# Performance work log

Hardware: AMD Instinct MI355X
Metric: run time of the kernel (lower is better)

## Reference

```python
import jax, jax.numpy as jnp
import numpy as np

B, T, E, H, V = 128, 400, 128, 128, 50000
H2, H4, H6 = 2 * H, 4 * H, 6 * H


def setup_inputs() -> dict:
    key = jax.random.key(0)
    ks = jax.random.split(key, 16)
    s = 0.05
    return dict(
        input_ids=jax.random.randint(ks[0], (B, 1), 0, V),
        pre_hidden=jax.random.normal(ks[1], (1, B, H2), jnp.float32),
        pre_cell=jax.random.normal(ks[2], (1, B, H2), jnp.float32),
        enc_outputs=jax.random.normal(ks[3], (B, T, H2), jnp.float32),
        source_input=jax.random.randint(ks[4], (B, T), 0, V),
        coverage=jax.random.uniform(ks[5], (B, 1, T), jnp.float32),
        emb_table=s * jax.random.normal(ks[6], (V, E), jnp.float32),
        w_ih=s * jax.random.normal(ks[7], (4 * H2, E), jnp.float32),
        w_hh=s * jax.random.normal(ks[8], (4 * H2, H2), jnp.float32),
        b_ih=jnp.zeros((4 * H2,), jnp.float32),
        b_hh=jnp.zeros((4 * H2,), jnp.float32),
        w_align=s * jax.random.normal(ks[9], (1, H6), jnp.float32),
        b_align=jnp.zeros((1,), jnp.float32),
        w_cov=s * jax.random.normal(ks[10], (H2, 1), jnp.float32),
        b_cov=jnp.zeros((H2,), jnp.float32),
        w_fc1=s * jax.random.normal(ks[11], (H4, H4), jnp.float32),
        b_fc1=jnp.zeros((H4,), jnp.float32),
        w_fc2=s * jax.random.normal(ks[12], (V, H4), jnp.float32),
        b_fc2=jnp.zeros((V,), jnp.float32),
        w_gen=s * jax.random.normal(ks[13], (1, H4 + E), jnp.float32),
        b_gen=jnp.zeros((1,), jnp.float32),
    )


def reference(input_ids, pre_hidden, pre_cell, enc_outputs, source_input, coverage,
              emb_table, w_ih, w_hh, b_ih, b_hh, w_align, b_align, w_cov, b_cov,
              w_fc1, b_fc1, w_fc2, b_fc2, w_gen, b_gen):
    # embedding lookup (flag=False path: no dropout)
    emb = emb_table[input_ids[:, 0]]                      # [B,E]
    # single-step LSTM (PyTorch gate order i,f,g,o; hidden size 2H)
    h0, c0 = pre_hidden[0], pre_cell[0]                   # [B,2H]
    gates = emb @ w_ih.T + b_ih + h0 @ w_hh.T + b_hh      # [B,8H]
    i, f, g, o = jnp.split(gates, 4, axis=-1)
    c = jax.nn.sigmoid(f) * c0 + jax.nn.sigmoid(i) * jnp.tanh(g)
    h = jax.nn.sigmoid(o) * jnp.tanh(c)                   # [B,2H]
    # coverage feature + attention over encoder steps
    cov_feat = coverage.transpose(0, 2, 1) @ w_cov.T + b_cov        # [B,T,2H]
    h_rep = jnp.broadcast_to(h[:, None, :], enc_outputs.shape)     # [B,T,2H]
    combine = jnp.concatenate([enc_outputs, h_rep, cov_feat], -1)  # [B,T,6H]
    scores = jnp.tanh(combine @ w_align.T + b_align)               # [B,T,1]
    attn = jax.nn.softmax(scores, axis=1)                          # [B,T,1]
    attn_bt = attn[:, :, 0]                                        # [B,T]
    cov_bt = coverage[:, 0, :]
    cov_loss = jnp.sum(jnp.minimum(attn_bt, cov_bt))
    new_cov = coverage + attn_bt[:, None, :]                       # [B,1,T]
    # context + vocab distribution
    context = jnp.einsum('bt,bte->be', attn_bt, enc_outputs)       # [B,2H]
    fc = jnp.tanh(jnp.concatenate([h, context], -1) @ w_fc1.T + b_fc1)
    pvocab = jax.nn.softmax(fc @ w_fc2.T + b_fc2, axis=1)          # [B,V]
    # copy distribution: fused batched scatter-add (replaces per-batch one-hot matmul loop)
    b_idx = jnp.arange(attn_bt.shape[0])[:, None]
    copy = jnp.zeros_like(pvocab).at[b_idx, source_input].add(attn_bt)
    # generation probability and mixture
    gen_in = jnp.concatenate([context, h, emb], -1)                # [B,4H+E]
    pgen = jax.nn.sigmoid(gen_in @ w_gen.T + b_gen)                # [B,1]
    out = pvocab * pgen + copy * (1.0 - pgen)
    return (out, h[None], c[None], attn_bt[:, None, :], copy, new_cov, cov_loss)
```

## Files before the change

kernel.cpp:

```cpp
#include <hip/hip_runtime.h>
#include <hip/hip_bf16.h>
#include <math.h>

#define B_  128
#define T_  400
#define E_  128
#define H2_ 256
#define H4_ 512
#define V_  50000
#define G4_ 1024
#define KACT 384
#define NTILE 1563

#define OFF_H       6400000
#define OFF_C       6432768
#define OFF_ATTN    6465536
#define OFF_COPY    6516736
#define OFF_NEWCOV 12916736
#define OFF_COVLOSS 12967936

#define WS_ACT   0
#define WS_GATES (WS_ACT + KACT*B_)
#define WS_HC    (WS_GATES + G4_*B_)
#define WS_FCB   (WS_HC + H4_*B_)
#define WS_SC    (WS_FCB + H4_*B_/2)
#define WS_ATTN  (WS_SC + B_*T_)
#define WS_CTXP  (WS_ATTN + B_*T_)
#define WS_SMP   (WS_CTXP + B_*8*H2_)
#define WS_HDOT  (WS_SMP + B_*8*2)
#define WS_COVP  (WS_HDOT + B_)
#define WS_PGEN  (WS_COVP + B_)
#define WS_MAX   (WS_PGEN + B_)
#define WS_INV   (WS_MAX + B_)
#define WS_AB    (WS_INV + B_)

typedef __attribute__((ext_vector_type(8))) short bf16x8;
typedef __attribute__((ext_vector_type(4))) float f32x4;
typedef __attribute__((ext_vector_type(16))) float f32x16;

__device__ inline float sigmoidf_(float x){ return 1.f/(1.f+__expf(-x)); }

__device__ inline short f2bf(float x){
  __hip_bfloat16 h = __float2bfloat16(x);
  return *reinterpret_cast<short*>(&h);
}

__device__ inline float blk_reduce_sum(float v, float* red){
  int t = threadIdx.x;
  red[t] = v; __syncthreads();
  for (int s = 128; s > 0; s >>= 1){ if (t < s) red[t] += red[t+s]; __syncthreads(); }
  float r = red[0]; __syncthreads(); return r;
}
__device__ inline float blk_reduce_max(float v, float* red){
  int t = threadIdx.x;
  red[t] = v; __syncthreads();
  for (int s = 128; s > 0; s >>= 1){ if (t < s) red[t] = fmaxf(red[t], red[t+s]); __syncthreads(); }
  float r = red[0]; __syncthreads(); return r;
}

__global__ __launch_bounds__(256) void k_zero(float* __restrict__ p){
  size_t i = ((size_t)blockIdx.x*256 + threadIdx.x)*4;
  if (i < (size_t)B_*V_)
    *(float4*)&p[i] = make_float4(0.f,0.f,0.f,0.f);
}

__global__ __launch_bounds__(256) void k_act(const int* __restrict__ ids,
    const float* __restrict__ pre_h, const float* __restrict__ emb_table,
    const float* __restrict__ w_align, const float* __restrict__ w_cov,
    const float* __restrict__ b_cov, float* __restrict__ act,
    float* __restrict__ ab){
  __shared__ float red[256];
  int t = threadIdx.x;
  int idx = blockIdx.x*256 + t;
  int k = idx >> 7, b = idx & 127;
  float v = (k < E_) ? emb_table[(size_t)ids[b]*E_ + k]
                     : pre_h[b*H2_ + (k - E_)];
  act[idx] = v;
  if (blockIdx.x == 0) {
    float wa = w_align[2*H2_ + t];
    float alpha = blk_reduce_sum(w_cov[t]*wa, red);
    float beta  = blk_reduce_sum(b_cov[t]*wa, red);
    if (t == 0) { ab[0] = alpha; ab[1] = beta; }
  }
}

__global__ __launch_bounds__(256) void k_gates(const float* __restrict__ act,
    const float* __restrict__ w_ih, const float* __restrict__ w_hh,
    const float* __restrict__ b_ih, const float* __restrict__ b_hh,
    float* __restrict__ gates){
  __shared__ float wt[8][KACT];
  int t = threadIdx.x; int j0 = blockIdx.x*8;
  for (int idx = t; idx < 8*KACT; idx += 256) {
    int r = idx / KACT, k = idx % KACT;
    int j = j0 + r;
    wt[r][k] = (k < E_) ? w_ih[j*E_ + k] : w_hh[j*H2_ + (k - E_)];
  }
  __syncthreads();
  int jq = t >> 7, b = t & 127;
  float acc[4] = {0.f,0.f,0.f,0.f};
  for (int k = 0; k < KACT; ++k) {
    float a = act[k*B_ + b];
    #pragma unroll
    for (int jj = 0; jj < 4; ++jj) acc[jj] += wt[jq*4+jj][k]*a;
  }
  #pragma unroll
  for (int jj = 0; jj < 4; ++jj) {
    int j = j0 + jq*4 + jj;
    gates[j*B_ + b] = acc[jj] + b_ih[j] + b_hh[j];
  }
}

__global__ __launch_bounds__(256) void k_lstm(const float* __restrict__ gates,
    const float* __restrict__ pre_c, const float* __restrict__ w_align,
    float* __restrict__ o_h, float* __restrict__ o_c,
    float* __restrict__ hc, float* __restrict__ hdot){
  __shared__ float red[256];
  int b = blockIdx.x, k = threadIdx.x;
  float i_ = gates[(0*H2_ + k)*B_ + b];
  float f_ = gates[(1*H2_ + k)*B_ + b];
  float g_ = gates[(2*H2_ + k)*B_ + b];
  float o_ = gates[(3*H2_ + k)*B_ + b];
  float c = sigmoidf_(f_)*pre_c[b*H2_ + k] + sigmoidf_(i_)*tanhf(g_);
  float h = sigmoidf_(o_)*tanhf(c);
  o_h[b*H2_ + k] = h;
  o_c[b*H2_ + k] = c;
  hc[k*B_ + b] = h;
  float s = blk_reduce_sum(h * w_align[H2_ + k], red);
  if (k == 0) hdot[b] = s;
}

__global__ __launch_bounds__(256) void k_scores(const float* __restrict__ enc,
    const float* __restrict__ cov, const float* __restrict__ w_align,
    const float* __restrict__ b_align, const float* __restrict__ hdot,
    const float* __restrict__ ab, float* __restrict__ sc){
  int b = blockIdx.y, c = blockIdx.x;
  int t = threadIdx.x, wave = t >> 6, lane = t & 63;
  float4 wa4 = *(const float4*)&w_align[lane*4];
  float hd = hdot[b], alpha = ab[0], beta = ab[1], ba = b_align[0];
  int t0 = c*50;
  for (int tt = t0 + wave; tt < t0 + 50; tt += 4) {
    const float4* ep = (const float4*)&enc[((size_t)b*T_ + tt)*H2_];
    float4 e4 = ep[lane];
    float d = e4.x*wa4.x + e4.y*wa4.y + e4.z*wa4.z + e4.w*wa4.w;
    #pragma unroll
    for (int m = 32; m >= 1; m >>= 1) d += __shfl_xor(d, m);
    if (lane == 0)
      sc[b*T_ + tt] = tanhf(d + hd + alpha*cov[b*T_ + tt] + beta + ba);
  }
}

__global__ __launch_bounds__(256) void k_soft(const float* __restrict__ sc_in,
    const float* __restrict__ cov, const int* __restrict__ src,
    float* __restrict__ o_attn, float* __restrict__ o_newcov,
    float* __restrict__ o_copy, float* __restrict__ covp,
    float* __restrict__ attn_ws){
  __shared__ float red[256];
  int b = blockIdx.x, t = threadIdx.x;
  float x1 = sc_in[b*T_ + t];
  float x2 = (t + 256 < T_) ? sc_in[b*T_ + t + 256] : -1e30f;
  float mx = blk_reduce_max(fmaxf(x1, x2), red);
  float e1 = __expf(x1 - mx);
  float e2 = (t + 256 < T_) ? __expf(x2 - mx) : 0.f;
  float sum = blk_reduce_sum(e1 + e2, red);
  float inv = 1.f/sum;
  float cl;
  {
    float a1 = e1*inv; float c1 = cov[b*T_ + t];
    attn_ws[b*T_ + t] = a1;
    o_attn[b*T_ + t] = a1;
    o_newcov[b*T_ + t] = c1 + a1;
    atomicAdd(&o_copy[(size_t)b*V_ + src[b*T_ + t]], a1);
    cl = fminf(a1, c1);
  }
  if (t + 256 < T_) {
    float a2 = e2*inv; float c2 = cov[b*T_ + t + 256];
    attn_ws[b*T_ + t + 256] = a2;
    o_attn[b*T_ + t + 256] = a2;
    o_newcov[b*T_ + t + 256] = c2 + a2;
    atomicAdd(&o_copy[(size_t)b*V_ + src[b*T_ + t + 256]], a2);
    cl += fminf(a2, c2);
  }
  float clsum = blk_reduce_sum(cl, red);
  if (t == 0) covp[b] = clsum;
}

__global__ __launch_bounds__(256) void k_ctx(const float* __restrict__ enc,
    const float* __restrict__ attn_ws, float* __restrict__ ctxp){
  __shared__ float a_s[50];
  int b = blockIdx.y, c = blockIdx.x, e = threadIdx.x;
  int t0 = c*50;
  if (e < 50) a_s[e] = attn_ws[b*T_ + t0 + e];
  __syncthreads();
  float acc = 0.f;
  #pragma unroll 5
  for (int i = 0; i < 50; ++i)
    acc += a_s[i] * enc[((size_t)b*T_ + t0 + i)*H2_ + e];
  ctxp[((size_t)b*8 + c)*H2_ + e] = acc;
}

__global__ __launch_bounds__(256) void k_ctxpgen(const float* __restrict__ ctxp,
    const int* __restrict__ ids, const float* __restrict__ emb_table,
    const float* __restrict__ w_gen, const float* __restrict__ b_gen,
    float* __restrict__ hc, float* __restrict__ pgen){
  __shared__ float red[256];
  int b = blockIdx.x, t = threadIdx.x;
  float ctx = 0.f;
  #pragma unroll
  for (int c = 0; c < 8; ++c) ctx += ctxp[((size_t)b*8 + c)*H2_ + t];
  hc[(H2_ + t)*B_ + b] = ctx;
  float p = ctx*w_gen[t] + hc[t*B_ + b]*w_gen[H2_ + t];
  if (t < E_) p += emb_table[(size_t)ids[b]*E_ + t]*w_gen[2*H2_ + t];
  float s = blk_reduce_sum(p, red);
  if (t == 0) pgen[b] = sigmoidf_(s + b_gen[0]);
}

__global__ __launch_bounds__(256) void k_fc1(const float* __restrict__ hc,
    const float* __restrict__ w_fc1, const float* __restrict__ b_fc1,
    short* __restrict__ fcb){
  __shared__ float wt[16][H4_];
  int t = threadIdx.x; int j0 = blockIdx.x*16;
  for (int idx = t; idx < 16*H4_; idx += 256) {
    int r = idx >> 9, k = idx & 511;
    wt[r][k] = w_fc1[(j0 + r)*H4_ + k];
  }
  __syncthreads();
  int jq = t >> 7, b = t & 127;
  float acc[8] = {};
  for (int k = 0; k < H4_; ++k) {
    float a = hc[k*B_ + b];
    #pragma unroll
    for (int jj = 0; jj < 8; ++jj) acc[jj] += wt[jq*8+jj][k]*a;
  }
  bf16x8 pack;
  #pragma unroll
  for (int jj = 0; jj < 8; ++jj) {
    int j = j0 + jq*8 + jj;
    pack[jj] = f2bf(tanhf(acc[jj] + b_fc1[j]));
  }
  *(bf16x8*)&fcb[(size_t)b*H4_ + j0 + jq*8] = pack;
}

__global__ __launch_bounds__(256, 1) void k_gemv(const short* __restrict__ fcb,
    const float* __restrict__ w_fc2, const float* __restrict__ b_fc2,
    float* __restrict__ logits){
  __shared__ __attribute__((aligned(16))) char lds[131072];
  int t = threadIdx.x;
  int w = t >> 6, l = t & 63;
  int ln = l & 31, g2 = l >> 5;

  #pragma unroll
  for (int i = 0; i < 32; ++i) {
    int s = i*256 + t;
    int c = s >> 9, r = (s & 511) >> 2, sg = s & 3;
    bf16x8 d = *(const bf16x8*)&fcb[r*H4_ + c*32 + sg*8];
    *(bf16x8*)(lds + c*8192 + sg*2048 + (((r ^ (sg << 1)) & 127)*16)) = d;
  }
  __syncthreads();

  int wgid = blockIdx.x*4 + w;
  for (int tile = wgid; tile < NTILE; tile += 1024) {
    int v = tile*32 + ln;
    int vc = v < V_ ? v : V_ - 1;
    const float* wr = w_fc2 + (size_t)vc*H4_ + g2*8;
    f32x16 acc0 = {}, acc1 = {}, acc2 = {}, acc3 = {};
    #pragma unroll 8
    for (int ks = 0; ks < 32; ++ks) {
      float4 f0 = *(const float4*)(wr + ks*16);
      float4 f1 = *(const float4*)(wr + ks*16 + 4);
      bf16x8 bf;
      bf[0]=f2bf(f0.x); bf[1]=f2bf(f0.y); bf[2]=f2bf(f0.z); bf[3]=f2bf(f0.w);
      bf[4]=f2bf(f1.x); bf[5]=f2bf(f1.y); bf[6]=f2bf(f1.z); bf[7]=f2bf(f1.w);
      int sg = (ks & 1)*2 + g2;
      char* base = lds + (ks >> 1)*8192 + sg*2048;
      bf16x8 a0 = *(const bf16x8*)(base + ((( 0 + ln) ^ (sg << 1)) & 127)*16);
      bf16x8 a1 = *(const bf16x8*)(base + (((32 + ln) ^ (sg << 1)) & 127)*16);
      bf16x8 a2 = *(const bf16x8*)(base + (((64 + ln) ^ (sg << 1)) & 127)*16);
      bf16x8 a3 = *(const bf16x8*)(base + (((96 + ln) ^ (sg << 1)) & 127)*16);
      acc0 = __builtin_amdgcn_mfma_f32_32x32x16_bf16(a0, bf, acc0, 0, 0, 0);
      acc1 = __builtin_amdgcn_mfma_f32_32x32x16_bf16(a1, bf, acc1, 0, 0, 0);
      acc2 = __builtin_amdgcn_mfma_f32_32x32x16_bf16(a2, bf, acc2, 0, 0, 0);
      acc3 = __builtin_amdgcn_mfma_f32_32x32x16_bf16(a3, bf, acc3, 0, 0, 0);
    }
    if (v < V_) {
      float bias = b_fc2[v];
      #pragma unroll
      for (int r = 0; r < 16; ++r) {
        int brow = (r & 3) + 8*(r >> 2) + 4*g2;
        logits[(size_t)(brow)*V_ + v]      = acc0[r] + bias;
        logits[(size_t)(32 + brow)*V_ + v] = acc1[r] + bias;
        logits[(size_t)(64 + brow)*V_ + v] = acc2[r] + bias;
        logits[(size_t)(96 + brow)*V_ + v] = acc3[r] + bias;
      }
    }
  }
}

__global__ __launch_bounds__(256) void k_smp(const float* __restrict__ logits,
    float* __restrict__ smp){
  __shared__ float rm[256], rs[256];
  int b = blockIdx.y, c = blockIdx.x, t = threadIdx.x;
  int v0 = c*6250, v1 = v0 + 6250;
  float m = -1e30f, s = 0.f;
  for (int v = v0 + t; v < v1; v += 256) {
    float x = logits[(size_t)b*V_ + v];
    float nm = fmaxf(m, x);
    s = s*__expf(m - nm) + __expf(x - nm);
    m = nm;
  }
  rm[t] = m; rs[t] = s; __syncthreads();
  for (int k = 128; k > 0; k >>= 1) {
    if (t < k) {
      float m1 = rm[t], s1 = rs[t], m2 = rm[t+k], s2 = rs[t+k];
      float nm = fmaxf(m1, m2);
      rm[t] = nm; rs[t] = s1*__expf(m1-nm) + s2*__expf(m2-nm);
    }
    __syncthreads();
  }
  if (t == 0) { smp[(b*8+c)*2] = rm[0]; smp[(b*8+c)*2+1] = rs[0]; }
}

__global__ __launch_bounds__(128) void k_smred_cl(const float* __restrict__ smp,
    const float* __restrict__ covp, float* __restrict__ mx,
    float* __restrict__ inv, float* __restrict__ o_cl){
  __shared__ float red[128];
  int t = threadIdx.x;
  float m = -1e30f, s = 0.f;
  #pragma unroll
  for (int c = 0; c < 8; ++c) {
    float m2 = smp[(t*8+c)*2], s2 = smp[(t*8+c)*2+1];
    float nm = fmaxf(m, m2);
    s = s*__expf(m - nm) + s2*__expf(m2 - nm);
    m = nm;
  }
  mx[t] = m; inv[t] = 1.f/s;
  red[t] = covp[t]; __syncthreads();
  for (int k = 64; k > 0; k >>= 1){ if (t < k) red[t] += red[t+k]; __syncthreads(); }
  if (t == 0) o_cl[0] = red[0];
}

__global__ __launch_bounds__(256) void k_final(const float* __restrict__ copy,
    const float* __restrict__ mx, const float* __restrict__ inv_s,
    const float* __restrict__ pgen, float* __restrict__ out){
  size_t gid = (size_t)blockIdx.x*256 + threadIdx.x;
  int b = (int)(gid / (V_/4));
  int v = (int)(gid % (V_/4))*4;
  size_t idx = (size_t)b*V_ + v;
  float m = mx[b], is = inv_s[b], pg = pgen[b];
  float4 lg = *(const float4*)&out[idx];
  float4 cp = *(const float4*)&copy[idx];
  float4 o;
  o.x = __expf(lg.x - m)*is*pg + cp.x*(1.f - pg);
  o.y = __expf(lg.y - m)*is*pg + cp.y*(1.f - pg);
  o.z = __expf(lg.z - m)*is*pg + cp.z*(1.f - pg);
  o.w = __expf(lg.w - m)*is*pg + cp.w*(1.f - pg);
  *(float4*)&out[idx] = o;
}

extern "C" void kernel_launch(void* const* d_in, const int* in_sizes, int n_in,
                              void* d_out, int out_size, void* d_ws, size_t ws_size,
                              hipStream_t stream) {
  const int*   ids       = (const int*)  d_in[0];
  const float* pre_h     = (const float*)d_in[1];
  const float* pre_c     = (const float*)d_in[2];
  const float* enc       = (const float*)d_in[3];
  const int*   src       = (const int*)  d_in[4];
  const float* cov       = (const float*)d_in[5];
  const float* emb_table = (const float*)d_in[6];
  const float* w_ih      = (const float*)d_in[7];
  const float* w_hh      = (const float*)d_in[8];
  const float* b_ih      = (const float*)d_in[9];
  const float* b_hh      = (const float*)d_in[10];
  const float* w_align   = (const float*)d_in[11];
  const float* b_align   = (const float*)d_in[12];
  const float* w_cov     = (const float*)d_in[13];
  const float* b_cov     = (const float*)d_in[14];
  const float* w_fc1     = (const float*)d_in[15];
  const float* b_fc1     = (const float*)d_in[16];
  const float* w_fc2     = (const float*)d_in[17];
  const float* b_fc2     = (const float*)d_in[18];
  const float* w_gen     = (const float*)d_in[19];
  const float* b_gen     = (const float*)d_in[20];

  float* out = (float*)d_out;
  float* ws  = (float*)d_ws;

  float* o_out    = out;
  float* o_h      = out + OFF_H;
  float* o_c      = out + OFF_C;
  float* o_attn   = out + OFF_ATTN;
  float* o_copy   = out + OFF_COPY;
  float* o_newcov = out + OFF_NEWCOV;
  float* o_cl     = out + OFF_COVLOSS;

  k_zero <<<(B_*V_/4 + 255)/256, 256, 0, stream>>>(o_copy);
  k_act  <<<192, 256, 0, stream>>>(ids, pre_h, emb_table, w_align, w_cov, b_cov,
                                   ws + WS_ACT, ws + WS_AB);
  k_gates<<<128, 256, 0, stream>>>(ws + WS_ACT, w_ih, w_hh, b_ih, b_hh, ws + WS_GATES);
  k_lstm <<<128, 256, 0, stream>>>(ws + WS_GATES, pre_c, w_align, o_h, o_c,
                                   ws + WS_HC, ws + WS_HDOT);
  k_scores<<<dim3(8,128), 256, 0, stream>>>(enc, cov, w_align, b_align,
                                   ws + WS_HDOT, ws + WS_AB, ws + WS_SC);
  k_soft <<<128, 256, 0, stream>>>(ws + WS_SC, cov, src, o_attn, o_newcov, o_copy,
                                   ws + WS_COVP, ws + WS_ATTN);
  k_ctx  <<<dim3(8,128), 256, 0, stream>>>(enc, ws + WS_ATTN, ws + WS_CTXP);
  k_ctxpgen<<<128, 256, 0, stream>>>(ws + WS_CTXP, ids, emb_table, w_gen, b_gen,
                                   ws + WS_HC, ws + WS_PGEN);
  k_fc1  <<<32, 256, 0, stream>>>(ws + WS_HC, w_fc1, b_fc1, (short*)(ws + WS_FCB));
  k_gemv <<<256, 256, 0, stream>>>((const short*)(ws + WS_FCB),
                                   w_fc2, b_fc2, o_out);
  k_smp  <<<dim3(8,128), 256, 0, stream>>>(o_out, ws + WS_SMP);
  k_smred_cl<<<1, 128, 0, stream>>>(ws + WS_SMP, ws + WS_COVP,
                                   ws + WS_MAX, ws + WS_INV, o_cl);
  k_final<<<(int)(((size_t)B_*V_/4)/256), 256, 0, stream>>>(
      o_copy, ws + WS_MAX, ws + WS_INV, ws + WS_PGEN, o_out);
}
```

Measured before the change: 156.4 us.

## Restructure vocab GEMM into triple-buffered async global-to-LDS pipelined tiles

Replaces the persistent-block fc2 kernel, which staged all activations in LDS once and streamed fp32 weights straight into registers, with a grid of 391 blocks that each own 128 vocab rows. Each block streams K-chunks of both the bf16 activations and the fp32 weights into a triple-buffered LDS ring using direct global-to-LDS loads, with explicit waitcnt and barriers so loads overlap MFMA work. LDS use drops to 72KB, which allows two blocks per CU. The cost is that activations are reloaded per block, the schedule depends on hand-tuned vmcnt counts, and there are more barriers.

```diff
diff --git a/kernel.cpp b/kernel.cpp
--- a/kernel.cpp
+++ b/kernel.cpp
@@ -10,7 +10,6 @@
 #define V_  50000
 #define G4_ 1024
 #define KACT 384
-#define NTILE 1563
 
 #define OFF_H       6400000
 #define OFF_C       6432768
@@ -43,6 +42,12 @@
 __device__ inline short f2bf(float x){
   __hip_bfloat16 h = __float2bfloat16(x);
   return *reinterpret_cast<short*>(&h);
+}
+
+__device__ __forceinline__ void load_to_lds16(const void* g, void* l){
+  __builtin_amdgcn_global_load_lds(
+      (const __attribute__((address_space(1))) void*)g,
+      (__attribute__((address_space(3))) void*)l, 16, 0, 0);
 }
 
 __device__ inline float blk_reduce_sum(float v, float* red){
@@ -240,57 +245,107 @@
   *(bf16x8*)&fcb[(size_t)b*H4_ + j0 + jq*8] = pack;
 }
 
-__global__ __launch_bounds__(256, 1) void k_gemv(const short* __restrict__ fcb,
+__global__ __launch_bounds__(256, 2) void k_gemm2m(const short* __restrict__ fcb,
     const float* __restrict__ w_fc2, const float* __restrict__ b_fc2,
     float* __restrict__ logits){
-  __shared__ __attribute__((aligned(16))) char lds[131072];
+  __shared__ __attribute__((aligned(16))) char lds[73728];
   int t = threadIdx.x;
   int w = t >> 6, l = t & 63;
   int ln = l & 31, g2 = l >> 5;
-
+  int v0 = blockIdx.x*128;
+  int v = v0 + w*32 + ln;
+  int vl = w*32 + ln;
+  (void)vl;
+
+  const char* gsrc[6];
+  int cstride[6];
+  int lbase = w*6*1024;
   #pragma unroll
-  for (int i = 0; i < 32; ++i) {
-    int s = i*256 + t;
-    int c = s >> 9, r = (s & 511) >> 2, sg = s & 3;
-    bf16x8 d = *(const bf16x8*)&fcb[r*H4_ + c*32 + sg*8];
-    *(bf16x8*)(lds + c*8192 + sg*2048 + (((r ^ (sg << 1)) & 127)*16)) = d;
-  }
-  __syncthreads();
-
-  int wgid = blockIdx.x*4 + w;
-  for (int tile = wgid; tile < NTILE; tile += 1024) {
-    int v = tile*32 + ln;
-    int vc = v < V_ ? v : V_ - 1;
-    const float* wr = w_fc2 + (size_t)vc*H4_ + g2*8;
-    f32x16 acc0 = {}, acc1 = {}, acc2 = {}, acc3 = {};
-    #pragma unroll 8
-    for (int ks = 0; ks < 32; ++ks) {
-      float4 f0 = *(const float4*)(wr + ks*16);
-      float4 f1 = *(const float4*)(wr + ks*16 + 4);
-      bf16x8 bf;
-      bf[0]=f2bf(f0.x); bf[1]=f2bf(f0.y); bf[2]=f2bf(f0.z); bf[3]=f2bf(f0.w);
-      bf[4]=f2bf(f1.x); bf[5]=f2bf(f1.y); bf[6]=f2bf(f1.z); bf[7]=f2bf(f1.w);
-      int sg = (ks & 1)*2 + g2;
-      char* base = lds + (ks >> 1)*8192 + sg*2048;
-      bf16x8 a0 = *(const bf16x8*)(base + ((( 0 + ln) ^ (sg << 1)) & 127)*16);
-      bf16x8 a1 = *(const bf16x8*)(base + (((32 + ln) ^ (sg << 1)) & 127)*16);
-      bf16x8 a2 = *(const bf16x8*)(base + (((64 + ln) ^ (sg << 1)) & 127)*16);
-      bf16x8 a3 = *(const bf16x8*)(base + (((96 + ln) ^ (sg << 1)) & 127)*16);
-      acc0 = __builtin_amdgcn_mfma_f32_32x32x16_bf16(a0, bf, acc0, 0, 0, 0);
-      acc1 = __builtin_amdgcn_mfma_f32_32x32x16_bf16(a1, bf, acc1, 0, 0, 0);
-      acc2 = __builtin_amdgcn_mfma_f32_32x32x16_bf16(a2, bf, acc2, 0, 0, 0);
-      acc3 = __builtin_amdgcn_mfma_f32_32x32x16_bf16(a3, bf, acc3, 0, 0, 0);
+  for (int j = 0; j < 6; ++j) {
+    int g = (w*6 + j)*64 + l;
+    if (g < 512) {
+      int q = g >> 7, r = (g & 127) ^ ((q << 1) & 127);
+      gsrc[j] = (const char*)(fcb + r*H4_ + q*8);
+      cstride[j] = 64;
+    } else {
+      int s = g - 512;
+      int kg = s >> 7, row = (s & 127) ^ kg;
+      int vr = v0 + row; if (vr >= V_) vr = V_ - 1;
+      gsrc[j] = (const char*)(w_fc2 + (size_t)vr*H4_ + kg*4);
+      cstride[j] = 128;
     }
-    if (v < V_) {
-      float bias = b_fc2[v];
-      #pragma unroll
-      for (int r = 0; r < 16; ++r) {
-        int brow = (r & 3) + 8*(r >> 2) + 4*g2;
-        logits[(size_t)(brow)*V_ + v]      = acc0[r] + bias;
-        logits[(size_t)(32 + brow)*V_ + v] = acc1[r] + bias;
-        logits[(size_t)(64 + brow)*V_ + v] = acc2[r] + bias;
-        logits[(size_t)(96 + brow)*V_ + v] = acc3[r] + bias;
-      }
+  }
+
+  f32x16 acc0 = {}, acc1 = {}, acc2 = {}, acc3 = {};
+
+  #define ISSUE(c, bi) {                                                      \
+    char* bb = lds + (bi)*24576;                                              \
+    _Pragma("unroll")                                                         \
+    for (int j = 0; j < 6; ++j)                                               \
+      load_to_lds16(gsrc[j] + (c)*cstride[j], bb + lbase + j*1024);           \
+    __builtin_amdgcn_sched_barrier(0);                                        \
+  }
+  #define COMPUTE(c) {                                                        \
+    char* Ab = lds + ((c) % 3)*24576;                                         \
+    char* Wb = Ab + 8192;                                                     \
+    _Pragma("unroll")                                                         \
+    for (int s = 0; s < 2; ++s) {                                             \
+      int sg = s*2 + g2;                                                      \
+      bf16x8 a0 = *(const bf16x8*)(Ab + sg*2048 + ((( 0+ln) ^ (sg<<1)) & 127)*16); \
+      bf16x8 a1 = *(const bf16x8*)(Ab + sg*2048 + (((32+ln) ^ (sg<<1)) & 127)*16); \
+      bf16x8 a2 = *(const bf16x8*)(Ab + sg*2048 + (((64+ln) ^ (sg<<1)) & 127)*16); \
+      bf16x8 a3 = *(const bf16x8*)(Ab + sg*2048 + (((96+ln) ^ (sg<<1)) & 127)*16); \
+      int kgA = s*4 + g2*2;                                                   \
+      f32x4 f0 = *(const f32x4*)(Wb + kgA*2048 + (((w*32+ln) ^ kgA) & 127)*16); \
+      int kgB = kgA + 1;                                                      \
+      f32x4 f1 = *(const f32x4*)(Wb + kgB*2048 + (((w*32+ln) ^ kgB) & 127)*16); \
+      bf16x8 bf;                                                              \
+      bf[0]=f2bf(f0[0]); bf[1]=f2bf(f0[1]); bf[2]=f2bf(f0[2]); bf[3]=f2bf(f0[3]); \
+      bf[4]=f2bf(f1[0]); bf[5]=f2bf(f1[1]); bf[6]=f2bf(f1[2]); bf[7]=f2bf(f1[3]); \
+      acc0 = __builtin_amdgcn_mfma_f32_32x32x16_bf16(a0, bf, acc0, 0, 0, 0);  \
+      acc1 = __builtin_amdgcn_mfma_f32_32x32x16_bf16(a1, bf, acc1, 0, 0, 0);  \
+      acc2 = __builtin_amdgcn_mfma_f32_32x32x16_bf16(a2, bf, acc2, 0, 0, 0);  \
+      acc3 = __builtin_amdgcn_mfma_f32_32x32x16_bf16(a3, bf, acc3, 0, 0, 0);  \
+    }                                                                         \
+  }
+  #define STEP(c, n) {                                                        \
+    asm volatile("s_waitcnt vmcnt(" #n ")" ::: "memory");                     \
+    __builtin_amdgcn_s_barrier();                                             \
+    __builtin_amdgcn_sched_barrier(0);                                        \
+    COMPUTE(c)                                                                \
+    asm volatile("s_waitcnt lgkmcnt(0)" ::: "memory");                        \
+    __builtin_amdgcn_s_barrier();                                             \
+    __builtin_amdgcn_sched_barrier(0);                                        \
+    ISSUE((c)+3, (c)%3)                                                       \
+  }
+  #define STEPE(c, n) {                                                       \
+    asm volatile("s_waitcnt vmcnt(" #n ")" ::: "memory");                     \
+    __builtin_amdgcn_s_barrier();                                             \
+    __builtin_amdgcn_sched_barrier(0);                                        \
+    COMPUTE(c)                                                                \
+  }
+
+  ISSUE(0, 0) ISSUE(1, 1) ISSUE(2, 2)
+  STEP(0, 12)  STEP(1, 12)  STEP(2, 12)  STEP(3, 12)
+  STEP(4, 12)  STEP(5, 12)  STEP(6, 12)  STEP(7, 12)
+  STEP(8, 12)  STEP(9, 12)  STEP(10, 12) STEP(11, 12)
+  STEP(12, 12)
+  STEPE(13, 12) STEPE(14, 6) STEPE(15, 0)
+
+  #undef ISSUE
+  #undef COMPUTE
+  #undef STEP
+  #undef STEPE
+
+  if (v < V_) {
+    float bias = b_fc2[v];
+    #pragma unroll
+    for (int r = 0; r < 16; ++r) {
+      int brow = (r & 3) + 8*(r >> 2) + 4*g2;
+      logits[(size_t)(brow)*V_ + v]      = acc0[r] + bias;
+      logits[(size_t)(32 + brow)*V_ + v] = acc1[r] + bias;
+      logits[(size_t)(64 + brow)*V_ + v] = acc2[r] + bias;
+      logits[(size_t)(96 + brow)*V_ + v] = acc3[r] + bias;
     }
   }
 }
@@ -406,7 +461,7 @@
   k_ctxpgen<<<128, 256, 0, stream>>>(ws + WS_CTXP, ids, emb_table, w_gen, b_gen,
                                    ws + WS_HC, ws + WS_PGEN);
   k_fc1  <<<32, 256, 0, stream>>>(ws + WS_HC, w_fc1, b_fc1, (short*)(ws + WS_FCB));
-  k_gemv <<<256, 256, 0, stream>>>((const short*)(ws + WS_FCB),
+  k_gemm2m<<<(V_ + 127)/128, 256, 0, stream>>>((const short*)(ws + WS_FCB),
                                    w_fc2, b_fc2, o_out);
   k_smp  <<<dim3(8,128), 256, 0, stream>>>(o_out, ws + WS_SMP);
   k_smred_cl<<<1, 128, 0, stream>>>(ws + WS_SMP, ws + WS_COVP,
```

After: 160.2 us. +2.4%, slower.
